# Optimization experiments

Measured on AMD Instinct MI355X. Metric: run time of the kernel, lower is better.

The kernel has to match this reference:

```python
import jax, jax.numpy as jnp
import numpy as np

P = 2  # sampling ratio: keep top ceil(M/p) measurements


def setup_inputs() -> dict:
    key = jax.random.key(0)
    k1, k2, k3 = jax.random.split(key, 3)
    B, H, W, C = 8, 1024, 1024, 3
    Y = jax.random.normal(k1, (B, H, W, C), dtype=jnp.float32)
    # build()-time Z0 components: abs ~ N(0.5, 0.1), angle ~ N(0, 0.5*sqrt(pi))
    Z0_abs = 0.5 + 0.1 * jax.random.normal(k2, (1, 1, H, W), dtype=jnp.float32)
    Z0_angle = (0.5 * np.pi ** 0.5) * jax.random.normal(k3, (1, 1, H, W), dtype=jnp.float32)
    return {"Y": Y, "Z0_abs": Z0_abs, "Z0_angle": Z0_angle}


def _make_Z0(Z0_abs, Z0_angle):
    # Z0 = |Z0| * exp(i*angle), Frobenius-normalized over spatial axes (2,3)
    Z0 = Z0_abs.astype(jnp.complex64) * jnp.exp(1j * Z0_angle.astype(jnp.complex64))
    fro = jnp.sqrt(jnp.sum(jnp.abs(Z0) ** 2, axis=(2, 3), keepdims=True)).astype(jnp.complex64)
    return Z0 / fro


def reference(Y, Z0_abs, Z0_angle):
    B, H, W, C = Y.shape
    M = H * W * C
    R = int(np.ceil(M / P))
    # transpose NHWC -> NCHW, scale by original S[2] (= W)
    Y_S = jnp.transpose(Y.astype(jnp.float32), (0, 3, 1, 2)) / jnp.float32(W)
    y_s = Y_S.reshape(B, M)
    # threshold = R-th largest value per batch (== descending-sorted index R-1)
    thr = jax.lax.top_k(y_s, R)[0][:, -1]  # [B]
    Ytr = (Y_S >= thr[:, None, None, None]).astype(jnp.float32)  # [B,C,H,W]
    Z0 = _make_Z0(Z0_abs, Z0_angle)
    return Ytr, Z0
```

## Files before the change

kernel.cpp:

```cpp
#include <hip/hip_runtime.h>
#include <math.h>

#define BATCH 8
#define HH 1024
#define WW 1024
#define CC 3
#define MTOT (HH*WW*CC)
#define RSEL 1572864u

#define NSEG2 256
#define LCAP 1024u
#define WCAP 131072u

#define U_HI 0xBC800000u
#define U_LO 0x437FFFFFu

#define WS_WCNT_OFF  0u
#define WS_CHI_OFF   64u
#define WS_NPART_OFF 256u
#define WS_THR_OFF   2048u
#define WS_NORM_OFF  2112u
#define WS_WBUF_OFF  4096u

__device__ __forceinline__ unsigned int fmap(float x) {
    unsigned int b = __float_as_uint(x);
    return (b & 0x80000000u) ? ~b : (b | 0x80000000u);
}

__global__ void pass1_kernel(const float* __restrict__ Y,
                             const float* __restrict__ zabs,
                             unsigned int* __restrict__ wbuf,
                             unsigned int* __restrict__ wcnt,
                             unsigned int* __restrict__ chib,
                             float* __restrict__ npart) {
    const int tid = threadIdx.x;
    const int bx = blockIdx.x;

    if (blockIdx.y == 8) {
        float s = 0.f;
        const int n4z = HH * WW / 4;
        for (int i = bx * 256 + tid; i < n4z; i += NSEG2 * 256) {
            float4 v = ((const float4*)zabs)[i];
            s += v.x * v.x + v.y * v.y + v.z * v.z + v.w * v.w;
        }
        for (int d = 32; d > 0; d >>= 1) s += __shfl_down(s, d);
        __shared__ float ls[4];
        if ((tid & 63) == 0) ls[tid >> 6] = s;
        __syncthreads();
        if (tid == 0) npart[bx] = ls[0] + ls[1] + ls[2] + ls[3];
        return;
    }

    __shared__ unsigned int lbuf[LCAP];
    __shared__ unsigned int lcnt;
    __shared__ unsigned int red[4];
    __shared__ unsigned int gbase_s;
    const int b = blockIdx.y;
    if (tid == 0) lcnt = 0u;
    __syncthreads();

    const float4* Y4 = (const float4*)(Y + (size_t)b * MTOT);
    const int stride = NSEG2 * 256;
    unsigned int hcnt = 0u;

#define PROC(c) do { unsigned int u = fmap(c); \
        if (u >= U_HI) hcnt++; \
        else if (u >= U_LO) { unsigned int p = atomicAdd(&lcnt, 1u); if (p < LCAP) lbuf[p] = u; } \
    } while (0)
#define PROC4(v) do { PROC(v.x); PROC(v.y); PROC(v.z); PROC(v.w); } while (0)

    for (int it = 0; it < 12; it += 4) {
        int i0 = it * stride + bx * 256 + tid;
        float4 v0 = Y4[i0];
        float4 v1 = Y4[i0 + stride];
        float4 v2 = Y4[i0 + 2 * stride];
        float4 v3 = Y4[i0 + 3 * stride];
        PROC4(v0); PROC4(v1); PROC4(v2); PROC4(v3);
    }
#undef PROC4
#undef PROC

    __syncthreads();
    unsigned int n = lcnt;
    unsigned int nc = (n > LCAP) ? LCAP : n;
    if (tid == 0) {
        unsigned int add = (n > LCAP) ? (WCAP + 1u) : n;
        gbase_s = atomicAdd(&wcnt[b], add);
    }
    for (int d = 32; d > 0; d >>= 1) hcnt += __shfl_down(hcnt, d);
    if ((tid & 63) == 0) red[tid >> 6] = hcnt;
    __syncthreads();
    if (tid == 0) atomicAdd(&chib[b], red[0] + red[1] + red[2] + red[3]);

    unsigned int gbase = gbase_s;
    unsigned int* wb = wbuf + (size_t)b * WCAP;
    for (unsigned int j = tid; j < nc; j += 256u) {
        unsigned int p = gbase + j;
        if (p < WCAP) wb[p] = lbuf[j];
    }
}

__global__ void __launch_bounds__(1024) refine_kernel(
        const float* __restrict__ Y,
        const unsigned int* __restrict__ wbuf,
        const unsigned int* __restrict__ wcnt,
        const unsigned int* __restrict__ chib,
        const float* __restrict__ npart,
        unsigned int* __restrict__ thr,
        float* __restrict__ normsum) {
    const int tid = threadIdx.x;

    if (blockIdx.x == 8) {
        float s = (tid < NSEG2) ? npart[tid] : 0.f;
        for (int d = 32; d > 0; d >>= 1) s += __shfl_down(s, d);
        __shared__ float ls[16];
        if ((tid & 63) == 0) ls[tid >> 6] = s;
        __syncthreads();
        if (tid == 0) {
            float t = 0.f;
            for (int i = 0; i < 16; i++) t += ls[i];
            *normsum = t;
        }
        return;
    }

    __shared__ unsigned int hist[4096];
    __shared__ unsigned int waveSums[16];
    __shared__ unsigned int selBin, selBase;
    const int b = blockIdx.x;
    const int lane = tid & 63, wid = tid >> 6;

    const unsigned int wc = wcnt[b];
    const unsigned int Ch = chib[b];
    const int fb = (wc > WCAP) || (Ch >= RSEL) || (Ch + wc < RSEL);
    unsigned int target = fb ? RSEL : (RSEL - Ch);
    const unsigned int wcg = (wc > WCAP) ? WCAP : wc;
    const unsigned int* wp = wbuf + (size_t)b * WCAP;
    const float* Yb = Y + (size_t)b * MTOT;

    unsigned int d1 = 0, d2 = 0;

    for (int level = 0; level < 3; level++) {
        const int nb  = (level < 2) ? 4096 : 256;
        const int bpt = (level < 2) ? 4 : 1;
        for (int i = tid; i < nb; i += 1024) hist[i] = 0u;
        if (tid == 0) { selBin = 0u; selBase = 0u; }
        __syncthreads();

#define HISTO(u) do { \
            if (level == 0) atomicAdd(&hist[(u) >> 20], 1u); \
            else if (level == 1) { if (((u) >> 20) == d1) atomicAdd(&hist[((u) >> 8) & 0xFFFu], 1u); } \
            else { if (((u) >> 8) == ((d1 << 12) | d2)) atomicAdd(&hist[(u) & 0xFFu], 1u); } \
        } while (0)

        if (fb) {
            for (unsigned int i = tid; i < (unsigned int)MTOT; i += 1024u) {
                unsigned int u = fmap(Yb[i]);
                HISTO(u);
            }
        } else {
            for (unsigned int i = tid; i < wcg; i += 1024u) {
                unsigned int u = wp[i];
                HISTO(u);
            }
        }
#undef HISTO
        __syncthreads();
        unsigned int c[4] = {0u, 0u, 0u, 0u};
        unsigned int s = 0u;
        const int nthr = nb / bpt;
        if (tid < nthr)
            for (int k = 0; k < bpt; k++) { c[k] = hist[nb - 1 - (tid * bpt + k)]; s += c[k]; }
        unsigned int incl = s;
        for (int d = 1; d < 64; d <<= 1) {
            unsigned int v = __shfl_up(incl, d);
            if (lane >= d) incl += v;
        }
        if (lane == 63) waveSums[wid] = incl;
        __syncthreads();
        if (tid < 16) {
            unsigned int w = waveSums[tid];
            for (int d = 1; d < 16; d <<= 1) {
                unsigned int v = __shfl_up(w, d);
                if (tid >= d) w += v;
            }
            waveSums[tid] = w;
        }
        __syncthreads();
        incl += (wid > 0) ? waveSums[wid - 1] : 0u;
        unsigned int excl = incl - s;
        if (s > 0u && excl < target && incl >= target) {
            unsigned int run = excl;
            for (int k = 0; k < bpt; k++) {
                if (run + c[k] >= target) {
                    selBin = (unsigned int)(nb - 1 - (tid * bpt + k));
                    selBase = run;
                    break;
                }
                run += c[k];
            }
        }
        __syncthreads();
        if (level == 0) d1 = selBin;
        else if (level == 1) d2 = selBin;
        target -= selBase;
        __syncthreads();
    }
    if (tid == 0) thr[b] = (d1 << 20) | (d2 << 8) | selBin;
}

__global__ void thresh_z_kernel(const float* __restrict__ Y,
                                const unsigned int* __restrict__ thr,
                                const float* __restrict__ zabs,
                                const float* __restrict__ zang,
                                const float* __restrict__ normsum,
                                float* __restrict__ out,
                                float* __restrict__ outz, int interleaved) {
    if (blockIdx.x < 8192) {
        int p = blockIdx.x * blockDim.x + threadIdx.x;
        int w4 = p & 255;
        int h  = (p >> 8) & 1023;
        int b  = p >> 18;
        unsigned int tu = thr[b];
        const float4* src = (const float4*)(Y + ((size_t)((b * HH + h) * WW) + (size_t)w4 * 4) * CC);
        float4 a0 = src[0], a1 = src[1], a2 = src[2];
        float4 r0, r1, r2;
        r0.x = (fmap(a0.x) >= tu) ? 1.f : 0.f;
        r0.y = (fmap(a0.w) >= tu) ? 1.f : 0.f;
        r0.z = (fmap(a1.z) >= tu) ? 1.f : 0.f;
        r0.w = (fmap(a2.y) >= tu) ? 1.f : 0.f;
        r1.x = (fmap(a0.y) >= tu) ? 1.f : 0.f;
        r1.y = (fmap(a1.x) >= tu) ? 1.f : 0.f;
        r1.z = (fmap(a1.w) >= tu) ? 1.f : 0.f;
        r1.w = (fmap(a2.z) >= tu) ? 1.f : 0.f;
        r2.x = (fmap(a0.z) >= tu) ? 1.f : 0.f;
        r2.y = (fmap(a1.y) >= tu) ? 1.f : 0.f;
        r2.z = (fmap(a2.x) >= tu) ? 1.f : 0.f;
        r2.w = (fmap(a2.w) >= tu) ? 1.f : 0.f;
        size_t base = ((size_t)(b * CC) * HH + h) * WW;
        ((float4*)(out + base))[w4]                        = r0;
        ((float4*)(out + base + (size_t)HH * WW))[w4]      = r1;
        ((float4*)(out + base + (size_t)2 * HH * WW))[w4]  = r2;
    } else {
        int i = (blockIdx.x - 8192) * blockDim.x + threadIdx.x;
        float inv = 1.0f / sqrtf(*normsum);
        float2 a = ((const float2*)zabs)[i];
        float2 g = ((const float2*)zang)[i];
        float s0, c0, s1, c1;
        __sincosf(g.x, &s0, &c0);
        __sincosf(g.y, &s1, &c1);
        if (interleaved) {
            float4 o;
            o.x = a.x * c0 * inv; o.y = a.x * s0 * inv;
            o.z = a.y * c1 * inv; o.w = a.y * s1 * inv;
            ((float4*)outz)[i] = o;
        } else {
            float2 o;
            o.x = a.x * c0 * inv; o.y = a.y * c1 * inv;
            ((float2*)outz)[i] = o;
        }
    }
}

extern "C" void kernel_launch(void* const* d_in, const int* in_sizes, int n_in,
                              void* d_out, int out_size, void* d_ws, size_t ws_size,
                              hipStream_t stream) {
    const float* Y    = (const float*)d_in[0];
    const float* zabs = (const float*)d_in[1];
    const float* zang = (const float*)d_in[2];
    float* out = (float*)d_out;

    unsigned char* ws = (unsigned char*)d_ws;
    unsigned int* wcnt  = (unsigned int*)(ws + WS_WCNT_OFF);
    unsigned int* chib  = (unsigned int*)(ws + WS_CHI_OFF);
    float*        npart = (float*)(ws + WS_NPART_OFF);
    unsigned int* thr   = (unsigned int*)(ws + WS_THR_OFF);
    float*        norm  = (float*)(ws + WS_NORM_OFF);
    unsigned int* wbuf  = (unsigned int*)(ws + WS_WBUF_OFF);

    hipMemsetAsync(ws, 0, 96, stream);

    dim3 g1(NSEG2, 9);
    pass1_kernel<<<g1, 256, 0, stream>>>(Y, zabs, wbuf, wcnt, chib, npart);
    refine_kernel<<<9, 1024, 0, stream>>>(Y, wbuf, wcnt, chib, npart, thr, norm);

    size_t zoff = (size_t)BATCH * CC * HH * WW;
    int zfloats = out_size - (int)zoff;
    int interleaved = (zfloats >= 2 * HH * WW) ? 1 : 0;
    thresh_z_kernel<<<8192 + 2048, 256, 0, stream>>>(
        Y, thr, zabs, zang, norm, out, out + zoff, interleaved);
}
```

Before: 241.7 us.

## Write speculative threshold mask in pass1 and fix up only candidate elements

```diff
diff --git a/kernel.cpp b/kernel.cpp
--- a/kernel.cpp
+++ b/kernel.cpp
@@ -8,38 +8,65 @@
 #define MTOT (HH*WW*CC)
 #define RSEL 1572864u
 
-#define NSEG2 256
-#define LCAP 1024u
 #define WCAP 131072u
+#define LCAP2 512u
 
 #define U_HI 0xBC800000u
 #define U_LO 0x437FFFFFu
 
 #define WS_WCNT_OFF  0u
-#define WS_CHI_OFF   64u
-#define WS_NPART_OFF 256u
+#define WS_CHI_OFF   512u
+#define WS_NPART_OFF 1024u
 #define WS_THR_OFF   2048u
-#define WS_NORM_OFF  2112u
-#define WS_WBUF_OFF  4096u
+#define WS_FB_OFF    2112u
+#define WS_NORM_OFF  2176u
+#define WS_WU_OFF    4096u
+#define WS_WP_OFF    4198400u
 
 __device__ __forceinline__ unsigned int fmap(float x) {
     unsigned int b = __float_as_uint(x);
     return (b & 0x80000000u) ? ~b : (b | 0x80000000u);
 }
 
+__device__ __forceinline__ void thresh_row_quad(const float* __restrict__ Yb,
+                                                float* __restrict__ outb,
+                                                int h, int w4, unsigned int tu) {
+    const float4* src = (const float4*)(Yb + ((size_t)h * WW + (size_t)w4 * 4) * CC);
+    float4 a0 = src[0], a1 = src[1], a2 = src[2];
+    float4 r0, r1, r2;
+    r0.x = (fmap(a0.x) >= tu) ? 1.f : 0.f;
+    r0.y = (fmap(a0.w) >= tu) ? 1.f : 0.f;
+    r0.z = (fmap(a1.z) >= tu) ? 1.f : 0.f;
+    r0.w = (fmap(a2.y) >= tu) ? 1.f : 0.f;
+    r1.x = (fmap(a0.y) >= tu) ? 1.f : 0.f;
+    r1.y = (fmap(a1.x) >= tu) ? 1.f : 0.f;
+    r1.z = (fmap(a1.w) >= tu) ? 1.f : 0.f;
+    r1.w = (fmap(a2.z) >= tu) ? 1.f : 0.f;
+    r2.x = (fmap(a0.z) >= tu) ? 1.f : 0.f;
+    r2.y = (fmap(a1.y) >= tu) ? 1.f : 0.f;
+    r2.z = (fmap(a2.x) >= tu) ? 1.f : 0.f;
+    r2.w = (fmap(a2.w) >= tu) ? 1.f : 0.f;
+    size_t base = (size_t)h * WW;
+    ((float4*)(outb + base))[w4]                        = r0;
+    ((float4*)(outb + base + (size_t)HH * WW))[w4]      = r1;
+    ((float4*)(outb + base + (size_t)2 * HH * WW))[w4]  = r2;
+}
+
 __global__ void pass1_kernel(const float* __restrict__ Y,
                              const float* __restrict__ zabs,
-                             unsigned int* __restrict__ wbuf,
+                             float* __restrict__ out,
+                             unsigned int* __restrict__ wu,
+                             unsigned int* __restrict__ wpos,
                              unsigned int* __restrict__ wcnt,
                              unsigned int* __restrict__ chib,
                              float* __restrict__ npart) {
     const int tid = threadIdx.x;
-    const int bx = blockIdx.x;
-
-    if (blockIdx.y == 8) {
+
+    if (blockIdx.x >= 8192) {
+        const int bx = blockIdx.x - 8192;
         float s = 0.f;
         const int n4z = HH * WW / 4;
-        for (int i = bx * 256 + tid; i < n4z; i += NSEG2 * 256) {
+        for (int i = bx * 256 + tid; i < n4z; i += 256 * 256) {
             float4 v = ((const float4*)zabs)[i];
             s += v.x * v.x + v.y * v.y + v.z * v.z + v.w * v.w;
         }
@@ -51,67 +78,80 @@
         return;
     }
 
-    __shared__ unsigned int lbuf[LCAP];
+    __shared__ unsigned int lu[LCAP2];
+    __shared__ unsigned int lp[LCAP2];
     __shared__ unsigned int lcnt;
     __shared__ unsigned int red[4];
     __shared__ unsigned int gbase_s;
-    const int b = blockIdx.y;
     if (tid == 0) lcnt = 0u;
     __syncthreads();
 
-    const float4* Y4 = (const float4*)(Y + (size_t)b * MTOT);
-    const int stride = NSEG2 * 256;
+    const int p  = blockIdx.x * 256 + tid;
+    const int w4 = p & 255;
+    const int h  = (p >> 8) & 1023;
+    const int b  = p >> 18;
+    const unsigned int rowbase = (unsigned int)h * WW + (unsigned int)w4 * 4;
+
+    const float4* src = (const float4*)(Y + ((size_t)b * MTOT) + ((size_t)h * WW + (size_t)w4 * 4) * CC);
+    float4 a0 = src[0], a1 = src[1], a2 = src[2];
     unsigned int hcnt = 0u;
-
-#define PROC(c) do { unsigned int u = fmap(c); \
+    float4 r0, r1, r2;
+
+#define SPEC(val, c, k, dst) do { \
+        unsigned int u = fmap(val); \
+        dst = (u >= U_HI) ? 1.f : 0.f; \
         if (u >= U_HI) hcnt++; \
-        else if (u >= U_LO) { unsigned int p = atomicAdd(&lcnt, 1u); if (p < LCAP) lbuf[p] = u; } \
+        else if (u >= U_LO) { \
+            unsigned int pp = atomicAdd(&lcnt, 1u); \
+            if (pp < LCAP2) { lu[pp] = u; lp[pp] = (unsigned int)((c) * HH * WW) + rowbase + (unsigned int)(k); } \
+        } \
     } while (0)
-#define PROC4(v) do { PROC(v.x); PROC(v.y); PROC(v.z); PROC(v.w); } while (0)
-
-    for (int it = 0; it < 12; it += 4) {
-        int i0 = it * stride + bx * 256 + tid;
-        float4 v0 = Y4[i0];
-        float4 v1 = Y4[i0 + stride];
-        float4 v2 = Y4[i0 + 2 * stride];
-        float4 v3 = Y4[i0 + 3 * stride];
-        PROC4(v0); PROC4(v1); PROC4(v2); PROC4(v3);
-    }
-#undef PROC4
-#undef PROC
+
+    SPEC(a0.x, 0, 0, r0.x); SPEC(a0.w, 0, 1, r0.y); SPEC(a1.z, 0, 2, r0.z); SPEC(a2.y, 0, 3, r0.w);
+    SPEC(a0.y, 1, 0, r1.x); SPEC(a1.x, 1, 1, r1.y); SPEC(a1.w, 1, 2, r1.z); SPEC(a2.z, 1, 3, r1.w);
+    SPEC(a0.z, 2, 0, r2.x); SPEC(a1.y, 2, 1, r2.y); SPEC(a2.x, 2, 2, r2.z); SPEC(a2.w, 2, 3, r2.w);
+#undef SPEC
+
+    float* outb = out + (size_t)b * MTOT;
+    size_t base = (size_t)h * WW;
+    ((float4*)(outb + base))[w4]                        = r0;
+    ((float4*)(outb + base + (size_t)HH * WW))[w4]      = r1;
+    ((float4*)(outb + base + (size_t)2 * HH * WW))[w4]  = r2;
 
     __syncthreads();
     unsigned int n = lcnt;
-    unsigned int nc = (n > LCAP) ? LCAP : n;
+    unsigned int nc = (n > LCAP2) ? LCAP2 : n;
     if (tid == 0) {
-        unsigned int add = (n > LCAP) ? (WCAP + 1u) : n;
-        gbase_s = atomicAdd(&wcnt[b], add);
+        unsigned int add = (n > LCAP2) ? (WCAP + 1u) : n;
+        gbase_s = atomicAdd(&wcnt[b * 16], add);
     }
     for (int d = 32; d > 0; d >>= 1) hcnt += __shfl_down(hcnt, d);
     if ((tid & 63) == 0) red[tid >> 6] = hcnt;
     __syncthreads();
-    if (tid == 0) atomicAdd(&chib[b], red[0] + red[1] + red[2] + red[3]);
+    if (tid == 0) atomicAdd(&chib[b * 16], red[0] + red[1] + red[2] + red[3]);
 
     unsigned int gbase = gbase_s;
-    unsigned int* wb = wbuf + (size_t)b * WCAP;
+    unsigned int* wub = wu + (size_t)b * WCAP;
+    unsigned int* wpb = wpos + (size_t)b * WCAP;
     for (unsigned int j = tid; j < nc; j += 256u) {
-        unsigned int p = gbase + j;
-        if (p < WCAP) wb[p] = lbuf[j];
+        unsigned int q = gbase + j;
+        if (q < WCAP) { wub[q] = lu[j]; wpb[q] = lp[j]; }
     }
 }
 
 __global__ void __launch_bounds__(1024) refine_kernel(
         const float* __restrict__ Y,
-        const unsigned int* __restrict__ wbuf,
+        const unsigned int* __restrict__ wu,
         const unsigned int* __restrict__ wcnt,
         const unsigned int* __restrict__ chib,
         const float* __restrict__ npart,
         unsigned int* __restrict__ thr,
+        unsigned int* __restrict__ fbflag,
         float* __restrict__ normsum) {
     const int tid = threadIdx.x;
 
     if (blockIdx.x == 8) {
-        float s = (tid < NSEG2) ? npart[tid] : 0.f;
+        float s = (tid < 256) ? npart[tid] : 0.f;
         for (int d = 32; d > 0; d >>= 1) s += __shfl_down(s, d);
         __shared__ float ls[16];
         if ((tid & 63) == 0) ls[tid >> 6] = s;
@@ -130,12 +170,12 @@
     const int b = blockIdx.x;
     const int lane = tid & 63, wid = tid >> 6;
 
-    const unsigned int wc = wcnt[b];
-    const unsigned int Ch = chib[b];
+    const unsigned int wc = wcnt[b * 16];
+    const unsigned int Ch = chib[b * 16];
     const int fb = (wc > WCAP) || (Ch >= RSEL) || (Ch + wc < RSEL);
     unsigned int target = fb ? RSEL : (RSEL - Ch);
     const unsigned int wcg = (wc > WCAP) ? WCAP : wc;
-    const unsigned int* wp = wbuf + (size_t)b * WCAP;
+    const unsigned int* wp = wu + (size_t)b * WCAP;
     const float* Yb = Y + (size_t)b * MTOT;
 
     unsigned int d1 = 0, d2 = 0;
@@ -206,43 +246,26 @@
         target -= selBase;
         __syncthreads();
     }
-    if (tid == 0) thr[b] = (d1 << 20) | (d2 << 8) | selBin;
-}
-
-__global__ void thresh_z_kernel(const float* __restrict__ Y,
-                                const unsigned int* __restrict__ thr,
-                                const float* __restrict__ zabs,
-                                const float* __restrict__ zang,
-                                const float* __restrict__ normsum,
-                                float* __restrict__ out,
-                                float* __restrict__ outz, int interleaved) {
-    if (blockIdx.x < 8192) {
-        int p = blockIdx.x * blockDim.x + threadIdx.x;
-        int w4 = p & 255;
-        int h  = (p >> 8) & 1023;
-        int b  = p >> 18;
-        unsigned int tu = thr[b];
-        const float4* src = (const float4*)(Y + ((size_t)((b * HH + h) * WW) + (size_t)w4 * 4) * CC);
-        float4 a0 = src[0], a1 = src[1], a2 = src[2];
-        float4 r0, r1, r2;
-        r0.x = (fmap(a0.x) >= tu) ? 1.f : 0.f;
-        r0.y = (fmap(a0.w) >= tu) ? 1.f : 0.f;
-        r0.z = (fmap(a1.z) >= tu) ? 1.f : 0.f;
-        r0.w = (fmap(a2.y) >= tu) ? 1.f : 0.f;
-        r1.x = (fmap(a0.y) >= tu) ? 1.f : 0.f;
-        r1.y = (fmap(a1.x) >= tu) ? 1.f : 0.f;
-        r1.z = (fmap(a1.w) >= tu) ? 1.f : 0.f;
-        r1.w = (fmap(a2.z) >= tu) ? 1.f : 0.f;
-        r2.x = (fmap(a0.z) >= tu) ? 1.f : 0.f;
-        r2.y = (fmap(a1.y) >= tu) ? 1.f : 0.f;
-        r2.z = (fmap(a2.x) >= tu) ? 1.f : 0.f;
-        r2.w = (fmap(a2.w) >= tu) ? 1.f : 0.f;
-        size_t base = ((size_t)(b * CC) * HH + h) * WW;
-        ((float4*)(out + base))[w4]                        = r0;
-        ((float4*)(out + base + (size_t)HH * WW))[w4]      = r1;
-        ((float4*)(out + base + (size_t)2 * HH * WW))[w4]  = r2;
-    } else {
-        int i = (blockIdx.x - 8192) * blockDim.x + threadIdx.x;
+    if (tid == 0) {
+        thr[b] = (d1 << 20) | (d2 << 8) | selBin;
+        fbflag[b] = (unsigned int)fb;
+    }
+}
+
+__global__ void fixup_z_kernel(const float* __restrict__ Y,
+                               const unsigned int* __restrict__ wu,
+                               const unsigned int* __restrict__ wpos,
+                               const unsigned int* __restrict__ wcnt,
+                               const unsigned int* __restrict__ thr,
+                               const unsigned int* __restrict__ fbflag,
+                               const float* __restrict__ zabs,
+                               const float* __restrict__ zang,
+                               const float* __restrict__ normsum,
+                               float* __restrict__ out,
+                               float* __restrict__ outz, int interleaved) {
+    const int tid = threadIdx.x;
+    if (blockIdx.x < 2048) {
+        int i = blockIdx.x * 256 + tid;
         float inv = 1.0f / sqrtf(*normsum);
         float2 a = ((const float2*)zabs)[i];
         float2 g = ((const float2*)zang)[i];
@@ -259,6 +282,27 @@
             o.x = a.x * c0 * inv; o.y = a.y * c1 * inv;
             ((float2*)outz)[i] = o;
         }
+    } else {
+        const int j = blockIdx.x - 2048;
+        const int b = j >> 8;
+        const unsigned int tu = thr[b];
+        float* outb = out + (size_t)b * MTOT;
+        if (fbflag[b]) {
+            const float* Yb = Y + (size_t)b * MTOT;
+            for (int q = (j & 255); q < 1024; q += 256) {
+                int pq = q * 256 + tid;
+                thresh_row_quad(Yb, outb, pq >> 8, pq & 255, tu);
+            }
+        } else {
+            const unsigned int wc = wcnt[b * 16];
+            const unsigned int* wub = wu + (size_t)b * WCAP;
+            const unsigned int* wpb = wpos + (size_t)b * WCAP;
+            for (unsigned int i = (unsigned int)(j & 255) * 256u + tid; i < wc; i += 65536u) {
+                unsigned int u = wub[i];
+                unsigned int pos = wpb[i];
+                outb[pos] = (u >= tu) ? 1.f : 0.f;
+            }
+        }
     }
 }
 
@@ -275,18 +319,19 @@
     unsigned int* chib  = (unsigned int*)(ws + WS_CHI_OFF);
     float*        npart = (float*)(ws + WS_NPART_OFF);
     unsigned int* thr   = (unsigned int*)(ws + WS_THR_OFF);
+    unsigned int* fbf   = (unsigned int*)(ws + WS_FB_OFF);
     float*        norm  = (float*)(ws + WS_NORM_OFF);
-    unsigned int* wbuf  = (unsigned int*)(ws + WS_WBUF_OFF);
-
-    hipMemsetAsync(ws, 0, 96, stream);
-
-    dim3 g1(NSEG2, 9);
-    pass1_kernel<<<g1, 256, 0, stream>>>(Y, zabs, wbuf, wcnt, chib, npart);
-    refine_kernel<<<9, 1024, 0, stream>>>(Y, wbuf, wcnt, chib, npart, thr, norm);
+    unsigned int* wu    = (unsigned int*)(ws + WS_WU_OFF);
+    unsigned int* wpos  = (unsigned int*)(ws + WS_WP_OFF);
+
+    hipMemsetAsync(ws, 0, 1024, stream);
+
+    pass1_kernel<<<8192 + 256, 256, 0, stream>>>(Y, zabs, out, wu, wpos, wcnt, chib, npart);
+    refine_kernel<<<9, 1024, 0, stream>>>(Y, wu, wcnt, chib, npart, thr, fbf, norm);
 
     size_t zoff = (size_t)BATCH * CC * HH * WW;
     int zfloats = out_size - (int)zoff;
     int interleaved = (zfloats >= 2 * HH * WW) ? 1 : 0;
-    thresh_z_kernel<<<8192 + 2048, 256, 0, stream>>>(
-        Y, thr, zabs, zang, norm, out, out + zoff, interleaved);
-}
+    fixup_z_kernel<<<2048 + 2048, 256, 0, stream>>>(
+        Y, wu, wpos, wcnt, thr, fbf, zabs, zang, norm, out, out + zoff, interleaved);
+}
```

After: 250.1 us. +3.5%, slower.
